# Optimization experiments

Hardware: AMD Instinct MI355X
Metric: run time of the kernel (lower is better)

## Reference

```python
import jax, jax.numpy as jnp
import numpy as np

N_HEAD = 16
HEAD_DIM = 64

def rotate_half(x):
    x1, x2 = jnp.split(x, 2, axis=-1)
    return jnp.concatenate((-x2, x1), axis=-1)

def rope_tables(T, dim):
    inv_freq = 1.0 / (10000.0 ** (jnp.arange(0, dim, 2, dtype=jnp.float32) / dim))
    t = jnp.arange(T, dtype=jnp.float32)
    freqs = jnp.einsum('i,j->ij', t, inv_freq)          # [T, dim/2]
    emb = jnp.concatenate((freqs, freqs), axis=-1)       # [T, dim]
    return jnp.cos(emb)[None, None], jnp.sin(emb)[None, None]  # [1,1,T,dim]

def setup_inputs() -> dict:
    key = jax.random.key(0)
    k1, k2, k3 = jax.random.split(key, 3)
    C = N_HEAD * HEAD_DIM
    x = jax.random.normal(k1, (2, 2048, C), dtype=jnp.float32)
    W_qkv = jax.random.normal(k2, (C, 3 * C), dtype=jnp.float32) * (1.0 / np.sqrt(C))
    W_proj = jax.random.normal(k3, (C, C), dtype=jnp.float32) * (1.0 / np.sqrt(C))
    return {"x": x, "W_qkv": W_qkv, "W_proj": W_proj}

def reference(x, W_qkv, W_proj):
    B, T, C = x.shape
    qkv = x @ W_qkv                                       # [B,T,3C]
    q, k, v = jnp.split(qkv, 3, axis=-1)
    def to_heads(a):
        return a.reshape(B, T, N_HEAD, HEAD_DIM).transpose(0, 2, 1, 3)  # [B,H,T,D]
    q, k, v = to_heads(q), to_heads(k), to_heads(v)
    cos, sin = rope_tables(T, HEAD_DIM)
    q = q * cos + rotate_half(q) * sin
    k = k * cos + rotate_half(k) * sin
    scale = 1.0 / jnp.sqrt(jnp.asarray(HEAD_DIM, dtype=x.dtype))
    scores = jnp.einsum('bhqd,bhkd->bhqk', q, k) * scale  # [B,H,T,T]
    causal = jnp.tril(jnp.ones((T, T), dtype=bool))
    scores = jnp.where(causal[None, None], scores, jnp.finfo(scores.dtype).min)
    attn = jax.nn.softmax(scores, axis=-1)
    out = jnp.einsum('bhqk,bhkd->bhqd', attn, v)          # [B,H,T,D]
    out = out.transpose(0, 2, 1, 3).reshape(B, T, C)
    return out @ W_proj
```

## Files before the change

kernel.cpp:

```cpp
#include <hip/hip_runtime.h>
#include <cstdint>
#include <cstddef>

typedef __attribute__((ext_vector_type(8))) short bf16x8;
typedef __attribute__((ext_vector_type(4))) float f32x4;

__device__ __forceinline__ unsigned short f2bf(float f) {
  unsigned int u = __builtin_bit_cast(unsigned int, f);
  u += 0x7FFFu + ((u >> 16) & 1u);
  return (unsigned short)(u >> 16);
}
__device__ __forceinline__ float bf2f(unsigned short h) {
  unsigned int u = ((unsigned int)h) << 16;
  return __builtin_bit_cast(float, u);
}

__device__ __forceinline__ void gl_lds16(const unsigned short* g, unsigned short* l) {
  __builtin_amdgcn_global_load_lds(
      (const __attribute__((address_space(1))) unsigned int*)(uintptr_t)g,
      (__attribute__((address_space(3))) unsigned int*)(unsigned int)(uintptr_t)l,
      16, 0, 0);
}

__global__ void k_prep(const float* __restrict__ x,
                       const float* __restrict__ Wqkv,
                       const float* __restrict__ Wproj,
                       unsigned short* __restrict__ xb,
                       unsigned short* __restrict__ wqt,
                       unsigned short* __restrict__ wpt,
                       float2* __restrict__ cstab) {
  __shared__ float tile[32][33];
  const int bid = blockIdx.x, tid = threadIdx.x;
  if (bid < 4096) {
    int i = bid * 256 + tid;
    float4 v = reinterpret_cast<const float4*>(x)[i];
    uint2 o;
    o.x = (unsigned int)f2bf(v.x) | ((unsigned int)f2bf(v.y) << 16);
    o.y = (unsigned int)f2bf(v.z) | ((unsigned int)f2bf(v.w) << 16);
    reinterpret_cast<uint2*>(xb)[i] = o;
  } else if (bid < 8192) {
    const float* in; unsigned short* out; int rows, cols, bx, by;
    if (bid < 7168) { in = Wqkv; out = wqt; rows = 1024; cols = 3072; bx = (bid - 4096) % 96; by = (bid - 4096) / 96; }
    else            { in = Wproj; out = wpt; rows = 1024; cols = 1024; bx = (bid - 7168) % 32; by = (bid - 7168) / 32; }
    int c0 = bx * 32, r0 = by * 32;
    int tx = tid & 31, ty = tid >> 5;
#pragma unroll
    for (int j = 0; j < 4; j++)
      tile[ty + j * 8][tx] = in[(size_t)(r0 + ty + j * 8) * cols + c0 + tx];
    __syncthreads();
#pragma unroll
    for (int j = 0; j < 4; j++)
      out[(size_t)(c0 + ty + j * 8) * rows + r0 + tx] = f2bf(tile[tx][ty + j * 8]);
  } else {
    int i = (bid - 8192) * 256 + tid;
    int t = i >> 5, j = i & 31;
    float invf = __powf(10000.0f, -(float)j / 32.0f);
    float ang = (float)t * invf;
    cstab[i] = make_float2(cosf(ang), sinf(ang));
  }
}

__global__ void k_gemm_qkv(const unsigned short* __restrict__ A,
                           const unsigned short* __restrict__ Bt,
                           const float2* __restrict__ cstab,
                           unsigned short* __restrict__ qh,
                           unsigned short* __restrict__ kh,
                           unsigned short* __restrict__ vt) {
  const int K = 1024;
  __shared__ unsigned short Ta[128 * 32];
  __shared__ unsigned short Tb[128 * 32];
  const int tid = threadIdx.x;
  const int bid0 = blockIdx.y * 24 + blockIdx.x;
  const int bid = (bid0 & 7) * 96 + (bid0 >> 3);
  const int m0 = (bid / 24) * 128, n0 = (bid % 24) * 128;
  const int w = tid >> 6, l = tid & 63;
  const int lr = l & 15, lg = l >> 4;
  const int wm = (w >> 1) * 64, wn = (w & 1) * 64;
  const int ssr = w * 32 + (l >> 2);
  const int ssc = (l & 3) * 8;
  unsigned short* ta0 = &Ta[w * 1024];
  unsigned short* tb0 = &Tb[w * 1024];
  f32x4 acc[4][4] = {};
  for (int k0 = 0; k0 < K; k0 += 32) {
    __syncthreads();
    gl_lds16(&A[(size_t)(m0 + ssr) * K + k0 + ssc],       ta0);
    gl_lds16(&A[(size_t)(m0 + ssr + 16) * K + k0 + ssc],  ta0 + 512);
    gl_lds16(&Bt[(size_t)(n0 + ssr) * K + k0 + ssc],      tb0);
    gl_lds16(&Bt[(size_t)(n0 + ssr + 16) * K + k0 + ssc], tb0 + 512);
    __syncthreads();
    bf16x8 af[4], bfr[4];
#pragma unroll
    for (int i = 0; i < 4; i++)
      af[i] = *(const bf16x8*)&Ta[(wm + i * 16 + lr) * 32 + lg * 8];
#pragma unroll
    for (int j = 0; j < 4; j++)
      bfr[j] = *(const bf16x8*)&Tb[(wn + j * 16 + lr) * 32 + lg * 8];
#pragma unroll
    for (int i = 0; i < 4; i++)
#pragma unroll
      for (int j = 0; j < 4; j++)
        acc[i][j] = __builtin_amdgcn_mfma_f32_16x16x32_bf16(af[i], bfr[j], acc[i][j], 0, 0, 0);
  }
  const int part = n0 >> 10;
  const int hbase = (n0 & 1023) + wn;
  if (part < 2) {
    unsigned short* dst = part ? kh : qh;
    const float scale = part ? 1.0f : 0.180336880111120420f;
#pragma unroll
    for (int i = 0; i < 4; i++) {
#pragma unroll
      for (int r = 0; r < 4; r++) {
        int gm = m0 + wm + i * 16 + lg * 4 + r;
        int t = gm & 2047, b = gm >> 11;
        float2 cs0 = cstab[t * 32 + lr];
        float2 cs1 = cstab[t * 32 + 16 + lr];
#pragma unroll
        for (int j = 0; j < 4; j++) {
          float val = acc[i][j][r];
          float par = acc[i][j ^ 2][r];
          float2 cs = (j & 1) ? cs1 : cs0;
          float out = (j < 2) ? (val * cs.x - par * cs.y)
                              : (val * cs.x + par * cs.y);
          int h = (hbase + j * 16) >> 6;
          int d = j * 16 + lr;
          int bh = b * 16 + h;
          dst[((size_t)(bh * 2048 + t)) * 64 + d] = f2bf(out * scale);
        }
      }
    }
  } else {
#pragma unroll
    for (int i = 0; i < 4; i++) {
      int tb = m0 + wm + i * 16 + lg * 4;
      int t0 = tb & 2047, b = tb >> 11;
#pragma unroll
      for (int j = 0; j < 4; j++) {
        int h = (hbase + j * 16) >> 6;
        int d = j * 16 + lr;
        int bh = b * 16 + h;
        unsigned short pv[4];
#pragma unroll
        for (int r = 0; r < 4; r++) pv[r] = f2bf(acc[i][j][r]);
        *(uint2*)&vt[((size_t)(bh * 64 + d)) * 2048 + t0] = *(uint2*)pv;
      }
    }
  }
}

__global__ void k_gemm_proj(const unsigned short* __restrict__ A,
                            const unsigned short* __restrict__ Bt,
                            float* __restrict__ C) {
  const int K = 1024;
  __shared__ unsigned short Ta[64 * 32];
  __shared__ unsigned short Tb[128 * 32];
  const int tid = threadIdx.x;
  const int bid0 = blockIdx.x;
  const int bid = (bid0 & 7) * 64 + (bid0 >> 3);
  const int n0 = (bid & 7) * 128;
  const int m0 = (bid >> 3) * 64;
  const int w = tid >> 6, l = tid & 63;
  const int lr = l & 15, lg = l >> 4;
  const int wn = w * 32;
  const int sra = tid >> 2, sca = (tid & 3) * 8;
  f32x4 acc[4][2] = {};
  for (int k0 = 0; k0 < K; k0 += 32) {
    __syncthreads();
    gl_lds16(&A[(size_t)(m0 + sra) * K + k0 + sca],        &Ta[tid * 8]);
    gl_lds16(&Bt[(size_t)(n0 + sra) * K + k0 + sca],       &Tb[tid * 8]);
    gl_lds16(&Bt[(size_t)(n0 + 64 + sra) * K + k0 + sca],  &Tb[(tid + 256) * 8]);
    __syncthreads();
    bf16x8 af[4], bfr[2];
#pragma unroll
    for (int i = 0; i < 4; i++)
      af[i] = *(const bf16x8*)&Ta[(i * 16 + lr) * 32 + lg * 8];
#pragma unroll
    for (int j = 0; j < 2; j++)
      bfr[j] = *(const bf16x8*)&Tb[(wn + j * 16 + lr) * 32 + lg * 8];
#pragma unroll
    for (int i = 0; i < 4; i++)
#pragma unroll
      for (int j = 0; j < 2; j++)
        acc[i][j] = __builtin_amdgcn_mfma_f32_16x16x32_bf16(af[i], bfr[j], acc[i][j], 0, 0, 0);
  }
#pragma unroll
  for (int i = 0; i < 4; i++)
#pragma unroll
    for (int j = 0; j < 2; j++)
#pragma unroll
      for (int r = 0; r < 4; r++)
        C[(size_t)(m0 + i * 16 + lg * 4 + r) * 1024 + n0 + wn + j * 16 + lr] = acc[i][j][r];
}

__global__ __launch_bounds__(256, 2) void k_attn(const unsigned short* __restrict__ qh,
                       const unsigned short* __restrict__ kh,
                       const unsigned short* __restrict__ vt,
                       unsigned short* __restrict__ att) {
  __shared__ unsigned short Kl[64 * 64];
  __shared__ unsigned short Vl[64 * 64];
  __shared__ unsigned short Pl[4][16 * 64];
  const int bid = blockIdx.x;
  const int bh  = ((bid & 7) << 2) | ((bid >> 3) >> 4);
  const int qt0 = (bid >> 3) & 15;
  const int qt1 = 31 - qt0;
  const int b = bh >> 4, h = bh & 15;
  const int tid = threadIdx.x;
  const int w = tid >> 6, l = tid & 63;
  const int lr = l & 15, lg = l >> 4;
  const unsigned short* qbase = qh + (size_t)bh * 2048 * 64;
  const unsigned short* kbase = kh + (size_t)bh * 2048 * 64;
  const unsigned short* vbase = vt + (size_t)bh * 64 * 2048;
  char* KB = (char*)Kl;
  char* VB = (char*)Vl;
  char* PB = (char*)&Pl[w][0];
  const int swz = (lr & 7) << 4;
  const int sr = tid >> 2, sc = (tid & 3) * 16;
  const int sb0 = (sr * 128 + sc * 2) ^ ((sr & 7) << 4);
  const int sb1 = (sr * 128 + sc * 2 + 16) ^ ((sr & 7) << 4);

  const int q00 = qt0 * 64, q01 = qt1 * 64;
  const int qrow0 = q00 + w * 16 + lr;
  const int qrow1 = q01 + w * 16 + lr;
  bf16x8 qa0 = *(const bf16x8*)&qbase[(size_t)qrow0 * 64 + lg * 8];
  bf16x8 qb0 = *(const bf16x8*)&qbase[(size_t)qrow0 * 64 + 32 + lg * 8];
  bf16x8 qa1 = *(const bf16x8*)&qbase[(size_t)qrow1 * 64 + lg * 8];
  bf16x8 qb1 = *(const bf16x8*)&qbase[(size_t)qrow1 * 64 + 32 + lg * 8];

  float mr0 = -3.0e38f, ls0 = 0.0f;
  float mr1 = -3.0e38f, ls1 = 0.0f;
  f32x4 of0[4] = {}, of1[4] = {};
  uint4 ka0, ka1, va0, va1;

  auto issue = [&](int kv0) {
    const unsigned short* ksrc = &kbase[(size_t)(kv0 + sr) * 64 + sc];
    const unsigned short* vsrc = &vbase[(size_t)sr * 2048 + kv0 + sc];
    ka0 = *(const uint4*)ksrc; ka1 = *(const uint4*)(ksrc + 8);
    va0 = *(const uint4*)vsrc; va1 = *(const uint4*)(vsrc + 8);
  };

  auto step = [&](f32x4 (&of)[4], float& mr, float& ls, bf16x8 qa, bf16x8 qb,
                  int qrow, int kv0, bool diag) {
    f32x4 s[4] = {};
    __builtin_amdgcn_s_setprio(1);
#pragma unroll
    for (int kq = 0; kq < 4; kq++) {
      bf16x8 kf0 = *(const bf16x8*)(KB + (((kq * 16 + lr) * 128 + lg * 16) ^ swz));
      bf16x8 kf1 = *(const bf16x8*)(KB + (((kq * 16 + lr) * 128 + 64 + lg * 16) ^ swz));
      s[kq] = __builtin_amdgcn_mfma_f32_16x16x32_bf16(kf0, qa, s[kq], 0, 0, 0);
      s[kq] = __builtin_amdgcn_mfma_f32_16x16x32_bf16(kf1, qb, s[kq], 0, 0, 0);
    }
    __builtin_amdgcn_s_setprio(0);
    if (diag) {
#pragma unroll
      for (int kq = 0; kq < 4; kq++)
#pragma unroll
        for (int r = 0; r < 4; r++)
          if (kv0 + kq * 16 + lg * 4 + r > qrow) s[kq][r] = -3.0e38f;
    }
    float pm = s[0][0];
#pragma unroll
    for (int kq = 0; kq < 4; kq++)
#pragma unroll
      for (int r = 0; r < 4; r++) pm = fmaxf(pm, s[kq][r]);
    pm = fmaxf(pm, __shfl_xor(pm, 16));
    pm = fmaxf(pm, __shfl_xor(pm, 32));
    float mnew = fmaxf(mr, pm);
    float alpha = __builtin_amdgcn_exp2f(mr - mnew);
    mr = mnew;
    float psum = 0.0f;
#pragma unroll
    for (int kq = 0; kq < 4; kq++)
#pragma unroll
      for (int r = 0; r < 4; r++) {
        float p = __builtin_amdgcn_exp2f(s[kq][r] - mnew);
        s[kq][r] = p;
        psum += p;
      }
    psum += __shfl_xor(psum, 16);
    psum += __shfl_xor(psum, 32);
    ls = ls * alpha + psum;
#pragma unroll
    for (int n = 0; n < 4; n++) {
      of[n][0] *= alpha; of[n][1] *= alpha; of[n][2] *= alpha; of[n][3] *= alpha;
    }
#pragma unroll
    for (int kq = 0; kq < 4; kq++) {
      uint2 pk;
      asm("v_cvt_pk_bf16_f32 %0, %1, %2" : "=v"(pk.x) : "v"(s[kq][0]), "v"(s[kq][1]));
      asm("v_cvt_pk_bf16_f32 %0, %1, %2" : "=v"(pk.y) : "v"(s[kq][2]), "v"(s[kq][3]));
      *(uint2*)(PB + ((lr * 128 + (kq * 16 + lg * 4) * 2) ^ swz)) = pk;
    }
    bf16x8 pb0 = *(const bf16x8*)(PB + ((lr * 128 + lg * 16) ^ swz));
    bf16x8 pb1 = *(const bf16x8*)(PB + ((lr * 128 + 64 + lg * 16) ^ swz));
    __builtin_amdgcn_s_setprio(1);
#pragma unroll
    for (int n = 0; n < 4; n++) {
      bf16x8 vf0 = *(const bf16x8*)(VB + (((n * 16 + lr) * 128 + lg * 16) ^ swz));
      bf16x8 vf1 = *(const bf16x8*)(VB + (((n * 16 + lr) * 128 + 64 + lg * 16) ^ swz));
      of[n] = __builtin_amdgcn_mfma_f32_16x16x32_bf16(vf0, pb0, of[n], 0, 0, 0);
      of[n] = __builtin_amdgcn_mfma_f32_16x16x32_bf16(vf1, pb1, of[n], 0, 0, 0);
    }
    __builtin_amdgcn_s_setprio(0);
  };

  issue(0);
  const int nkv0 = qt0 + 1;
  for (int s2 = 0; s2 < 33; s2++) {
    __syncthreads();
    *(uint4*)(KB + sb0) = ka0;  *(uint4*)(KB + sb1) = ka1;
    *(uint4*)(VB + sb0) = va0;  *(uint4*)(VB + sb1) = va1;
    __syncthreads();
    if (s2 < 32) {
      int ns = s2 + 1;
      issue(((ns < nkv0) ? ns : ns - nkv0) * 64);
    }
    if (s2 < nkv0) step(of0, mr0, ls0, qa0, qb0, qrow0, s2 * 64, s2 == qt0);
    else           step(of1, mr1, ls1, qa1, qb1, qrow1, (s2 - nkv0) * 64, s2 == 32);
  }

  auto store_half = [&](f32x4 (&of)[4], float ls, int q0) {
    float inv = 1.0f / ls;
#pragma unroll
    for (int n = 0; n < 4; n++) {
      uint2 pk;
      float o0 = of[n][0] * inv, o1 = of[n][1] * inv, o2 = of[n][2] * inv, o3 = of[n][3] * inv;
      asm("v_cvt_pk_bf16_f32 %0, %1, %2" : "=v"(pk.x) : "v"(o0), "v"(o1));
      asm("v_cvt_pk_bf16_f32 %0, %1, %2" : "=v"(pk.y) : "v"(o2), "v"(o3));
      *(uint2*)(PB + ((lr * 128 + (n * 16 + lg * 4) * 2) ^ swz)) = pk;
    }
    int r2 = l >> 2, c2 = (l & 3) * 16;
    int bo0 = (r2 * 128 + c2 * 2) ^ ((r2 & 7) << 4);
    int bo1 = (r2 * 128 + c2 * 2 + 16) ^ ((r2 & 7) << 4);
    uint4 o0 = *(const uint4*)(PB + bo0);
    uint4 o1 = *(const uint4*)(PB + bo1);
    unsigned short* orow = att + (size_t)(b * 2048 + q0 + w * 16 + r2) * 1024 + h * 64 + c2;
    *(uint4*)orow = o0;
    *(uint4*)(orow + 8) = o1;
  };
  store_half(of0, ls0, q00);
  store_half(of1, ls1, q01);
}

extern "C" void kernel_launch(void* const* d_in, const int* in_sizes, int n_in,
                              void* d_out, int out_size, void* d_ws, size_t ws_size,
                              hipStream_t stream) {
  const float* x     = (const float*)d_in[0];
  const float* Wqkv  = (const float*)d_in[1];
  const float* Wproj = (const float*)d_in[2];
  float* out = (float*)d_out;

  char* ws = (char*)d_ws;
  size_t off = 0;
  auto alloc = [&](size_t bytes) { void* p = ws + off; off += (bytes + 255) & ~(size_t)255; return p; };
  unsigned short* xb   = (unsigned short*)alloc((size_t)4096 * 1024 * 2);
  unsigned short* wqt  = (unsigned short*)alloc((size_t)3072 * 1024 * 2);
  unsigned short* wpt  = (unsigned short*)alloc((size_t)1024 * 1024 * 2);
  unsigned short* qh   = (unsigned short*)alloc((size_t)32 * 2048 * 64 * 2);
  unsigned short* kh   = (unsigned short*)alloc((size_t)32 * 2048 * 64 * 2);
  unsigned short* vt   = (unsigned short*)alloc((size_t)32 * 64 * 2048 * 2);
  unsigned short* att  = (unsigned short*)alloc((size_t)4096 * 1024 * 2);
  float2* cstab = (float2*)alloc((size_t)2048 * 32 * 8);

  k_prep<<<8448, 256, 0, stream>>>(x, Wqkv, Wproj, xb, wqt, wpt, cstab);
  k_gemm_qkv<<<dim3(24, 32), 256, 0, stream>>>(xb, wqt, cstab, qh, kh, vt);
  k_attn<<<512, 256, 0, stream>>>(qh, kh, vt, att);
  k_gemm_proj<<<512, 256, 0, stream>>>(att, wpt, out);
}
```

Measured before the change: 105.0 us.

## Restructure attention kernel around 32x32 MFMA tiles with double-buffered K/V

The attention kernel now gives each wave 32 query rows, so a block covers a 128-row query tile, and it uses 32x32x16 bf16 MFMAs in place of 16x16x32 ones. The P matrix is transposed in registers with permlane32_swap instead of a round trip through LDS. K/V tiles are double-buffered in LDS, cutting one of the two barriers per iteration. The online softmax skips rescaling the accumulators when the running max does not change. The query-tile-to-block mapping drops the old pairing of short and long causal tiles for a per-XCD ordering, which risks load imbalance and higher register pressure from the 16-wide accumulators.

```diff
diff --git a/kernel.cpp b/kernel.cpp
--- a/kernel.cpp
+++ b/kernel.cpp
@@ -4,6 +4,8 @@
 
 typedef __attribute__((ext_vector_type(8))) short bf16x8;
 typedef __attribute__((ext_vector_type(4))) float f32x4;
+typedef __attribute__((ext_vector_type(16))) float f32x16;
+typedef __attribute__((ext_vector_type(2))) unsigned int uint32x2;
 
 __device__ __forceinline__ unsigned short f2bf(float f) {
   unsigned int u = __builtin_bit_cast(unsigned int, f);
@@ -13,6 +15,11 @@
 __device__ __forceinline__ float bf2f(unsigned short h) {
   unsigned int u = ((unsigned int)h) << 16;
   return __builtin_bit_cast(float, u);
+}
+__device__ __forceinline__ unsigned cvtpk(float a, float b) {
+  unsigned r;
+  asm("v_cvt_pk_bf16_f32 %0, %1, %2" : "=v"(r) : "v"(a), "v"(b));
+  return r;
 }
 
 __device__ __forceinline__ void gl_lds16(const unsigned short* g, unsigned short* l) {
@@ -195,39 +202,35 @@
                        const unsigned short* __restrict__ kh,
                        const unsigned short* __restrict__ vt,
                        unsigned short* __restrict__ att) {
-  __shared__ unsigned short Kl[64 * 64];
-  __shared__ unsigned short Vl[64 * 64];
-  __shared__ unsigned short Pl[4][16 * 64];
+  __shared__ char SMEM[32768];
   const int bid = blockIdx.x;
-  const int bh  = ((bid & 7) << 2) | ((bid >> 3) >> 4);
-  const int qt0 = (bid >> 3) & 15;
-  const int qt1 = 31 - qt0;
+  const int xcd = bid & 7, u = bid >> 3;
+  int hl, qt;
+  if (u < 32) { hl = u >> 3; qt = u & 7; }
+  else        { hl = (u - 32) >> 3; qt = 15 - ((u - 32) & 7); }
+  const int bh = xcd * 4 + hl;
   const int b = bh >> 4, h = bh & 15;
   const int tid = threadIdx.x;
   const int w = tid >> 6, l = tid & 63;
-  const int lr = l & 15, lg = l >> 4;
+  const int lq = l & 31, g = l >> 5;
   const unsigned short* qbase = qh + (size_t)bh * 2048 * 64;
   const unsigned short* kbase = kh + (size_t)bh * 2048 * 64;
   const unsigned short* vbase = vt + (size_t)bh * 64 * 2048;
-  char* KB = (char*)Kl;
-  char* VB = (char*)Vl;
-  char* PB = (char*)&Pl[w][0];
-  const int swz = (lr & 7) << 4;
+  const int swz = (lq & 7) << 4;
   const int sr = tid >> 2, sc = (tid & 3) * 16;
   const int sb0 = (sr * 128 + sc * 2) ^ ((sr & 7) << 4);
   const int sb1 = (sr * 128 + sc * 2 + 16) ^ ((sr & 7) << 4);
 
-  const int q00 = qt0 * 64, q01 = qt1 * 64;
-  const int qrow0 = q00 + w * 16 + lr;
-  const int qrow1 = q01 + w * 16 + lr;
-  bf16x8 qa0 = *(const bf16x8*)&qbase[(size_t)qrow0 * 64 + lg * 8];
-  bf16x8 qb0 = *(const bf16x8*)&qbase[(size_t)qrow0 * 64 + 32 + lg * 8];
-  bf16x8 qa1 = *(const bf16x8*)&qbase[(size_t)qrow1 * 64 + lg * 8];
-  bf16x8 qb1 = *(const bf16x8*)&qbase[(size_t)qrow1 * 64 + 32 + lg * 8];
-
-  float mr0 = -3.0e38f, ls0 = 0.0f;
-  float mr1 = -3.0e38f, ls1 = 0.0f;
-  f32x4 of0[4] = {}, of1[4] = {};
+  const int q0 = qt * 128;
+  const int wq = q0 + 32 * w;
+  const int qrow = wq + lq;
+  bf16x8 qf[4];
+#pragma unroll
+  for (int dt = 0; dt < 4; dt++)
+    qf[dt] = *(const bf16x8*)&qbase[(size_t)qrow * 64 + dt * 16 + g * 8];
+
+  float mr = -3.0e38f, ls = 0.0f;
+  f32x16 of0 = {}, of1 = {};
   uint4 ka0, ka1, va0, va1;
 
   auto issue = [&](int kv0) {
@@ -237,107 +240,123 @@
     va0 = *(const uint4*)vsrc; va1 = *(const uint4*)(vsrc + 8);
   };
 
-  auto step = [&](f32x4 (&of)[4], float& mr, float& ls, bf16x8 qa, bf16x8 qb,
-                  int qrow, int kv0, bool diag) {
-    f32x4 s[4] = {};
-    __builtin_amdgcn_s_setprio(1);
-#pragma unroll
-    for (int kq = 0; kq < 4; kq++) {
-      bf16x8 kf0 = *(const bf16x8*)(KB + (((kq * 16 + lr) * 128 + lg * 16) ^ swz));
-      bf16x8 kf1 = *(const bf16x8*)(KB + (((kq * 16 + lr) * 128 + 64 + lg * 16) ^ swz));
-      s[kq] = __builtin_amdgcn_mfma_f32_16x16x32_bf16(kf0, qa, s[kq], 0, 0, 0);
-      s[kq] = __builtin_amdgcn_mfma_f32_16x16x32_bf16(kf1, qb, s[kq], 0, 0, 0);
-    }
-    __builtin_amdgcn_s_setprio(0);
-    if (diag) {
-#pragma unroll
-      for (int kq = 0; kq < 4; kq++)
-#pragma unroll
-        for (int r = 0; r < 4; r++)
-          if (kv0 + kq * 16 + lg * 4 + r > qrow) s[kq][r] = -3.0e38f;
-    }
-    float pm = s[0][0];
-#pragma unroll
-    for (int kq = 0; kq < 4; kq++)
-#pragma unroll
-      for (int r = 0; r < 4; r++) pm = fmaxf(pm, s[kq][r]);
-    pm = fmaxf(pm, __shfl_xor(pm, 16));
-    pm = fmaxf(pm, __shfl_xor(pm, 32));
-    float mnew = fmaxf(mr, pm);
-    float alpha = __builtin_amdgcn_exp2f(mr - mnew);
-    mr = mnew;
-    float psum = 0.0f;
-#pragma unroll
-    for (int kq = 0; kq < 4; kq++)
-#pragma unroll
-      for (int r = 0; r < 4; r++) {
-        float p = __builtin_amdgcn_exp2f(s[kq][r] - mnew);
-        s[kq][r] = p;
-        psum += p;
-      }
-    psum += __shfl_xor(psum, 16);
-    psum += __shfl_xor(psum, 32);
-    ls = ls * alpha + psum;
-#pragma unroll
-    for (int n = 0; n < 4; n++) {
-      of[n][0] *= alpha; of[n][1] *= alpha; of[n][2] *= alpha; of[n][3] *= alpha;
-    }
-#pragma unroll
-    for (int kq = 0; kq < 4; kq++) {
-      uint2 pk;
-      asm("v_cvt_pk_bf16_f32 %0, %1, %2" : "=v"(pk.x) : "v"(s[kq][0]), "v"(s[kq][1]));
-      asm("v_cvt_pk_bf16_f32 %0, %1, %2" : "=v"(pk.y) : "v"(s[kq][2]), "v"(s[kq][3]));
-      *(uint2*)(PB + ((lr * 128 + (kq * 16 + lg * 4) * 2) ^ swz)) = pk;
-    }
-    bf16x8 pb0 = *(const bf16x8*)(PB + ((lr * 128 + lg * 16) ^ swz));
-    bf16x8 pb1 = *(const bf16x8*)(PB + ((lr * 128 + 64 + lg * 16) ^ swz));
-    __builtin_amdgcn_s_setprio(1);
-#pragma unroll
-    for (int n = 0; n < 4; n++) {
-      bf16x8 vf0 = *(const bf16x8*)(VB + (((n * 16 + lr) * 128 + lg * 16) ^ swz));
-      bf16x8 vf1 = *(const bf16x8*)(VB + (((n * 16 + lr) * 128 + 64 + lg * 16) ^ swz));
-      of[n] = __builtin_amdgcn_mfma_f32_16x16x32_bf16(vf0, pb0, of[n], 0, 0, 0);
-      of[n] = __builtin_amdgcn_mfma_f32_16x16x32_bf16(vf1, pb1, of[n], 0, 0, 0);
-    }
-    __builtin_amdgcn_s_setprio(0);
-  };
-
+  const int nkv = 2 * qt + 2;
   issue(0);
-  const int nkv0 = qt0 + 1;
-  for (int s2 = 0; s2 < 33; s2++) {
-    __syncthreads();
-    *(uint4*)(KB + sb0) = ka0;  *(uint4*)(KB + sb1) = ka1;
-    *(uint4*)(VB + sb0) = va0;  *(uint4*)(VB + sb1) = va1;
-    __syncthreads();
-    if (s2 < 32) {
-      int ns = s2 + 1;
-      issue(((ns < nkv0) ? ns : ns - nkv0) * 64);
-    }
-    if (s2 < nkv0) step(of0, mr0, ls0, qa0, qb0, qrow0, s2 * 64, s2 == qt0);
-    else           step(of1, mr1, ls1, qa1, qb1, qrow1, (s2 - nkv0) * 64, s2 == 32);
-  }
-
-  auto store_half = [&](f32x4 (&of)[4], float ls, int q0) {
-    float inv = 1.0f / ls;
-#pragma unroll
-    for (int n = 0; n < 4; n++) {
-      uint2 pk;
-      float o0 = of[n][0] * inv, o1 = of[n][1] * inv, o2 = of[n][2] * inv, o3 = of[n][3] * inv;
-      asm("v_cvt_pk_bf16_f32 %0, %1, %2" : "=v"(pk.x) : "v"(o0), "v"(o1));
-      asm("v_cvt_pk_bf16_f32 %0, %1, %2" : "=v"(pk.y) : "v"(o2), "v"(o3));
-      *(uint2*)(PB + ((lr * 128 + (n * 16 + lg * 4) * 2) ^ swz)) = pk;
-    }
-    int r2 = l >> 2, c2 = (l & 3) * 16;
-    int bo0 = (r2 * 128 + c2 * 2) ^ ((r2 & 7) << 4);
-    int bo1 = (r2 * 128 + c2 * 2 + 16) ^ ((r2 & 7) << 4);
-    uint4 o0 = *(const uint4*)(PB + bo0);
-    uint4 o1 = *(const uint4*)(PB + bo1);
-    unsigned short* orow = att + (size_t)(b * 2048 + q0 + w * 16 + r2) * 1024 + h * 64 + c2;
-    *(uint4*)orow = o0;
-    *(uint4*)(orow + 8) = o1;
-  };
-  store_half(of0, ls0, q00);
-  store_half(of1, ls1, q01);
+  {
+    char* KB0 = SMEM;
+    char* VB0 = SMEM + 8192;
+    *(uint4*)(KB0 + sb0) = ka0;  *(uint4*)(KB0 + sb1) = ka1;
+    *(uint4*)(VB0 + sb0) = va0;  *(uint4*)(VB0 + sb1) = va1;
+  }
+  __syncthreads();
+
+  for (int t = 0; t < nkv; t++) {
+    const int kv0 = t * 64;
+    char* KBc = SMEM + (t & 1) * 16384;
+    char* VBc = KBc + 8192;
+    if (t + 1 < nkv) issue(kv0 + 64);
+    if (kv0 <= wq + 31) {
+      f32x16 s0 = {}, s1 = {};
+      __builtin_amdgcn_s_setprio(1);
+#pragma unroll
+      for (int dt = 0; dt < 4; dt++) {
+        bf16x8 k0 = *(const bf16x8*)(KBc + lq * 128 + ((dt * 32 + g * 16) ^ swz));
+        bf16x8 k1 = *(const bf16x8*)(KBc + (32 + lq) * 128 + ((dt * 32 + g * 16) ^ swz));
+        s0 = __builtin_amdgcn_mfma_f32_32x32x16_bf16(k0, qf[dt], s0, 0, 0, 0);
+        s1 = __builtin_amdgcn_mfma_f32_32x32x16_bf16(k1, qf[dt], s1, 0, 0, 0);
+      }
+      __builtin_amdgcn_s_setprio(0);
+      if (kv0 + 63 > wq) {
+#pragma unroll
+        for (int r = 0; r < 16; r++) {
+          int kk = kv0 + (r & 3) + 8 * (r >> 2) + 4 * g;
+          if (kk > qrow)      s0[r] = -3.0e38f;
+          if (kk + 32 > qrow) s1[r] = -3.0e38f;
+        }
+      }
+      float pm = s0[0];
+#pragma unroll
+      for (int r = 1; r < 16; r++) pm = fmaxf(pm, s0[r]);
+#pragma unroll
+      for (int r = 0; r < 16; r++) pm = fmaxf(pm, s1[r]);
+      pm = fmaxf(pm, __shfl_xor(pm, 32));
+      if (__all(pm <= mr)) {
+        float psum = 0.0f;
+#pragma unroll
+        for (int r = 0; r < 16; r++) { float p = __builtin_amdgcn_exp2f(s0[r] - mr); s0[r] = p; psum += p; }
+#pragma unroll
+        for (int r = 0; r < 16; r++) { float p = __builtin_amdgcn_exp2f(s1[r] - mr); s1[r] = p; psum += p; }
+        psum += __shfl_xor(psum, 32);
+        ls += psum;
+      } else {
+        float mnew = fmaxf(mr, pm);
+        float alpha = __builtin_amdgcn_exp2f(mr - mnew);
+        mr = mnew;
+        float psum = 0.0f;
+#pragma unroll
+        for (int r = 0; r < 16; r++) { float p = __builtin_amdgcn_exp2f(s0[r] - mnew); s0[r] = p; psum += p; }
+#pragma unroll
+        for (int r = 0; r < 16; r++) { float p = __builtin_amdgcn_exp2f(s1[r] - mnew); s1[r] = p; psum += p; }
+        psum += __shfl_xor(psum, 32);
+        ls = ls * alpha + psum;
+        of0 = of0 * alpha;
+        of1 = of1 * alpha;
+      }
+      bf16x8 pf[4];
+#pragma unroll
+      for (int kt = 0; kt < 2; kt++) {
+        f32x16& s = kt ? s1 : s0;
+        unsigned x0 = cvtpk(s[0], s[1]),   x1 = cvtpk(s[2], s[3]);
+        unsigned x2 = cvtpk(s[4], s[5]),   x3 = cvtpk(s[6], s[7]);
+        unsigned y0 = cvtpk(s[8], s[9]),   y1 = cvtpk(s[10], s[11]);
+        unsigned y2 = cvtpk(s[12], s[13]), y3 = cvtpk(s[14], s[15]);
+        uint32x2 r02 = __builtin_amdgcn_permlane32_swap(x0, x2, false, false);
+        uint32x2 r13 = __builtin_amdgcn_permlane32_swap(x1, x3, false, false);
+        uint32x2 t02 = __builtin_amdgcn_permlane32_swap(y0, y2, false, false);
+        uint32x2 t13 = __builtin_amdgcn_permlane32_swap(y1, y3, false, false);
+        uint4 pa, pb2;
+        pa.x = r02[0]; pa.y = r13[0]; pa.z = r02[1]; pa.w = r13[1];
+        pb2.x = t02[0]; pb2.y = t13[0]; pb2.z = t02[1]; pb2.w = t13[1];
+        pf[kt * 2]     = __builtin_bit_cast(bf16x8, pa);
+        pf[kt * 2 + 1] = __builtin_bit_cast(bf16x8, pb2);
+      }
+      __builtin_amdgcn_s_setprio(1);
+#pragma unroll
+      for (int ks = 0; ks < 4; ks++) {
+        bf16x8 v0 = *(const bf16x8*)(VBc + lq * 128 + ((ks * 32 + g * 16) ^ swz));
+        bf16x8 v1 = *(const bf16x8*)(VBc + (32 + lq) * 128 + ((ks * 32 + g * 16) ^ swz));
+        of0 = __builtin_amdgcn_mfma_f32_32x32x16_bf16(v0, pf[ks], of0, 0, 0, 0);
+        of1 = __builtin_amdgcn_mfma_f32_32x32x16_bf16(v1, pf[ks], of1, 0, 0, 0);
+      }
+      __builtin_amdgcn_s_setprio(0);
+    }
+    if (t + 1 < nkv) {
+      char* KBn = SMEM + ((t + 1) & 1) * 16384;
+      char* VBn = KBn + 8192;
+      *(uint4*)(KBn + sb0) = ka0;  *(uint4*)(KBn + sb1) = ka1;
+      *(uint4*)(VBn + sb0) = va0;  *(uint4*)(VBn + sb1) = va1;
+    }
+    __syncthreads();
+  }
+
+  char* SB = SMEM + w * 4096;
+  float inv = 1.0f / ls;
+#pragma unroll
+  for (int j = 0; j < 8; j++) {
+    int d0 = ((2 * j) & 3) + 8 * (j >> 1) + 4 * g;
+    *(unsigned*)(SB + ((lq * 128 + d0 * 2) ^ swz)) = cvtpk(of0[2 * j] * inv, of0[2 * j + 1] * inv);
+    *(unsigned*)(SB + ((lq * 128 + (32 + d0) * 2) ^ swz)) = cvtpk(of1[2 * j] * inv, of1[2 * j + 1] * inv);
+  }
+  {
+    int r2 = l >> 1, half = l & 1;
+    int X = (r2 & 7) << 4;
+    unsigned short* orow = att + (size_t)(b * 2048 + wq + r2) * 1024 + h * 64 + half * 32;
+#pragma unroll
+    for (int i = 0; i < 4; i++) {
+      uint4 o = *(const uint4*)(SB + ((r2 * 128 + half * 64 + i * 16) ^ X));
+      *(uint4*)(orow + i * 8) = o;
+    }
+  }
 }
 
 extern "C" void kernel_launch(void* const* d_in, const int* in_sizes, int n_in,
```

After: 115.0 us. +9.6%, slower.

## Double-buffer K/V tiles in LDS and skip rescale when running max unchanged

Applied to the files above, without the earlier changes.

The attention kernel now keeps two LDS buffers for K and V. The next tile is written into the alternate buffer after the current tile's compute, which cuts the per-iteration syncs from two to one. Separately, the online softmax checks wave-wide whether the block max exceeds the running max, and skips the alpha exp and the output rescale when it does not. LDS use grows to 40 KB per block, which may limit occupancy under launch_bounds(256,2), and the branch adds wave-uniform control flow.

```diff
diff --git a/kernel.cpp b/kernel.cpp
--- a/kernel.cpp
+++ b/kernel.cpp
@@ -195,9 +195,7 @@
                        const unsigned short* __restrict__ kh,
                        const unsigned short* __restrict__ vt,
                        unsigned short* __restrict__ att) {
-  __shared__ unsigned short Kl[64 * 64];
-  __shared__ unsigned short Vl[64 * 64];
-  __shared__ unsigned short Pl[4][16 * 64];
+  __shared__ char SMEM[40960];
   const int bid = blockIdx.x;
   const int bh  = ((bid & 7) << 2) | ((bid >> 3) >> 4);
   const int qt0 = (bid >> 3) & 15;
@@ -209,9 +207,7 @@
   const unsigned short* qbase = qh + (size_t)bh * 2048 * 64;
   const unsigned short* kbase = kh + (size_t)bh * 2048 * 64;
   const unsigned short* vbase = vt + (size_t)bh * 64 * 2048;
-  char* KB = (char*)Kl;
-  char* VB = (char*)Vl;
-  char* PB = (char*)&Pl[w][0];
+  char* PB = SMEM + 32768 + w * 2048;
   const int swz = (lr & 7) << 4;
   const int sr = tid >> 2, sc = (tid & 3) * 16;
   const int sb0 = (sr * 128 + sc * 2) ^ ((sr & 7) << 4);
@@ -238,7 +234,7 @@
   };
 
   auto step = [&](f32x4 (&of)[4], float& mr, float& ls, bf16x8 qa, bf16x8 qb,
-                  int qrow, int kv0, bool diag) {
+                  int qrow, int kv0, bool diag, char* KB, char* VB) {
     f32x4 s[4] = {};
     __builtin_amdgcn_s_setprio(1);
 #pragma unroll
@@ -263,24 +259,38 @@
       for (int r = 0; r < 4; r++) pm = fmaxf(pm, s[kq][r]);
     pm = fmaxf(pm, __shfl_xor(pm, 16));
     pm = fmaxf(pm, __shfl_xor(pm, 32));
-    float mnew = fmaxf(mr, pm);
-    float alpha = __builtin_amdgcn_exp2f(mr - mnew);
-    mr = mnew;
     float psum = 0.0f;
-#pragma unroll
-    for (int kq = 0; kq < 4; kq++)
-#pragma unroll
-      for (int r = 0; r < 4; r++) {
-        float p = __builtin_amdgcn_exp2f(s[kq][r] - mnew);
-        s[kq][r] = p;
-        psum += p;
+    if (__all(pm <= mr)) {
+#pragma unroll
+      for (int kq = 0; kq < 4; kq++)
+#pragma unroll
+        for (int r = 0; r < 4; r++) {
+          float p = __builtin_amdgcn_exp2f(s[kq][r] - mr);
+          s[kq][r] = p;
+          psum += p;
+        }
+      psum += __shfl_xor(psum, 16);
+      psum += __shfl_xor(psum, 32);
+      ls += psum;
+    } else {
+      float mnew = fmaxf(mr, pm);
+      float alpha = __builtin_amdgcn_exp2f(mr - mnew);
+      mr = mnew;
+#pragma unroll
+      for (int kq = 0; kq < 4; kq++)
+#pragma unroll
+        for (int r = 0; r < 4; r++) {
+          float p = __builtin_amdgcn_exp2f(s[kq][r] - mnew);
+          s[kq][r] = p;
+          psum += p;
+        }
+      psum += __shfl_xor(psum, 16);
+      psum += __shfl_xor(psum, 32);
+      ls = ls * alpha + psum;
+#pragma unroll
+      for (int n = 0; n < 4; n++) {
+        of[n][0] *= alpha; of[n][1] *= alpha; of[n][2] *= alpha; of[n][3] *= alpha;
       }
-    psum += __shfl_xor(psum, 16);
-    psum += __shfl_xor(psum, 32);
-    ls = ls * alpha + psum;
-#pragma unroll
-    for (int n = 0; n < 4; n++) {
-      of[n][0] *= alpha; of[n][1] *= alpha; of[n][2] *= alpha; of[n][3] *= alpha;
     }
 #pragma unroll
     for (int kq = 0; kq < 4; kq++) {
@@ -302,19 +312,32 @@
     __builtin_amdgcn_s_setprio(0);
   };
 
+  const int nkv0 = qt0 + 1;
   issue(0);
-  const int nkv0 = qt0 + 1;
+  {
+    char* KB0 = SMEM;
+    char* VB0 = SMEM + 16384;
+    *(uint4*)(KB0 + sb0) = ka0;  *(uint4*)(KB0 + sb1) = ka1;
+    *(uint4*)(VB0 + sb0) = va0;  *(uint4*)(VB0 + sb1) = va1;
+  }
+  __syncthreads();
+
   for (int s2 = 0; s2 < 33; s2++) {
-    __syncthreads();
-    *(uint4*)(KB + sb0) = ka0;  *(uint4*)(KB + sb1) = ka1;
-    *(uint4*)(VB + sb0) = va0;  *(uint4*)(VB + sb1) = va1;
-    __syncthreads();
     if (s2 < 32) {
       int ns = s2 + 1;
       issue(((ns < nkv0) ? ns : ns - nkv0) * 64);
     }
-    if (s2 < nkv0) step(of0, mr0, ls0, qa0, qb0, qrow0, s2 * 64, s2 == qt0);
-    else           step(of1, mr1, ls1, qa1, qb1, qrow1, (s2 - nkv0) * 64, s2 == 32);
+    char* KB = SMEM + (s2 & 1) * 8192;
+    char* VB = SMEM + 16384 + (s2 & 1) * 8192;
+    if (s2 < nkv0) step(of0, mr0, ls0, qa0, qb0, qrow0, s2 * 64, s2 == qt0, KB, VB);
+    else           step(of1, mr1, ls1, qa1, qb1, qrow1, (s2 - nkv0) * 64, s2 == 32, KB, VB);
+    if (s2 < 32) {
+      char* KBn = SMEM + ((s2 + 1) & 1) * 8192;
+      char* VBn = SMEM + 16384 + ((s2 + 1) & 1) * 8192;
+      *(uint4*)(KBn + sb0) = ka0;  *(uint4*)(KBn + sb1) = ka1;
+      *(uint4*)(VBn + sb0) = va0;  *(uint4*)(VBn + sb1) = va1;
+    }
+    __syncthreads();
   }
 
   auto store_half = [&](f32x4 (&of)[4], float ls, int q0) {
```

Result: slower. 107.1 us (+2.0%).

## Split paired causal query tiles into separate blocks with balanced scheduling order

Applied to the files above, without the earlier changes.

Each attention block previously handled two query tiles (qt and 31-qt) so that every block did 33 KV steps. Now each block handles one query tile, the grid doubles to 1024, and occupancy is raised to four blocks per CU. A per-XCD ordering interleaves long and short tiles so the load still balances. This trades perfectly balanced per-block work for more parallelism and fewer registers, at the risk of tail imbalance and more redundant K/V loads.

```diff
diff --git a/kernel.cpp b/kernel.cpp
--- a/kernel.cpp
+++ b/kernel.cpp
@@ -191,7 +191,7 @@
         C[(size_t)(m0 + i * 16 + lg * 4 + r) * 1024 + n0 + wn + j * 16 + lr] = acc[i][j][r];
 }
 
-__global__ __launch_bounds__(256, 2) void k_attn(const unsigned short* __restrict__ qh,
+__global__ __launch_bounds__(256, 4) void k_attn(const unsigned short* __restrict__ qh,
                        const unsigned short* __restrict__ kh,
                        const unsigned short* __restrict__ vt,
                        unsigned short* __restrict__ att) {
@@ -199,9 +199,14 @@
   __shared__ unsigned short Vl[64 * 64];
   __shared__ unsigned short Pl[4][16 * 64];
   const int bid = blockIdx.x;
-  const int bh  = ((bid & 7) << 2) | ((bid >> 3) >> 4);
-  const int qt0 = (bid >> 3) & 15;
-  const int qt1 = 31 - qt0;
+  const int xcd = bid & 7, u = bid >> 3;
+  const int hl = u >> 5, v = u & 31;
+  int qt;
+  if      (hl == 0) qt = v;
+  else if (hl == 1) qt = 31 - v;
+  else if (hl == 2) qt = (v + 16) & 31;
+  else              qt = (47 - v) & 31;
+  const int bh = xcd * 4 + hl;
   const int b = bh >> 4, h = bh & 15;
   const int tid = threadIdx.x;
   const int w = tid >> 6, l = tid & 63;
@@ -217,17 +222,13 @@
   const int sb0 = (sr * 128 + sc * 2) ^ ((sr & 7) << 4);
   const int sb1 = (sr * 128 + sc * 2 + 16) ^ ((sr & 7) << 4);
 
-  const int q00 = qt0 * 64, q01 = qt1 * 64;
-  const int qrow0 = q00 + w * 16 + lr;
-  const int qrow1 = q01 + w * 16 + lr;
-  bf16x8 qa0 = *(const bf16x8*)&qbase[(size_t)qrow0 * 64 + lg * 8];
-  bf16x8 qb0 = *(const bf16x8*)&qbase[(size_t)qrow0 * 64 + 32 + lg * 8];
-  bf16x8 qa1 = *(const bf16x8*)&qbase[(size_t)qrow1 * 64 + lg * 8];
-  bf16x8 qb1 = *(const bf16x8*)&qbase[(size_t)qrow1 * 64 + 32 + lg * 8];
-
-  float mr0 = -3.0e38f, ls0 = 0.0f;
-  float mr1 = -3.0e38f, ls1 = 0.0f;
-  f32x4 of0[4] = {}, of1[4] = {};
+  const int q0 = qt * 64;
+  const int qrow = q0 + w * 16 + lr;
+  bf16x8 qa = *(const bf16x8*)&qbase[(size_t)qrow * 64 + lg * 8];
+  bf16x8 qb = *(const bf16x8*)&qbase[(size_t)qrow * 64 + 32 + lg * 8];
+
+  float mr = -3.0e38f, ls = 0.0f;
+  f32x4 of[4] = {};
   uint4 ka0, ka1, va0, va1;
 
   auto issue = [&](int kv0) {
@@ -237,8 +238,15 @@
     va0 = *(const uint4*)vsrc; va1 = *(const uint4*)(vsrc + 8);
   };
 
-  auto step = [&](f32x4 (&of)[4], float& mr, float& ls, bf16x8 qa, bf16x8 qb,
-                  int qrow, int kv0, bool diag) {
+  issue(0);
+  for (int kb = 0; kb <= qt; kb++) {
+    const int kv0 = kb * 64;
+    __syncthreads();
+    *(uint4*)(KB + sb0) = ka0;  *(uint4*)(KB + sb1) = ka1;
+    *(uint4*)(VB + sb0) = va0;  *(uint4*)(VB + sb1) = va1;
+    __syncthreads();
+    if (kb < qt) issue((kb + 1) * 64);
+
     f32x4 s[4] = {};
     __builtin_amdgcn_s_setprio(1);
 #pragma unroll
@@ -249,7 +257,7 @@
       s[kq] = __builtin_amdgcn_mfma_f32_16x16x32_bf16(kf1, qb, s[kq], 0, 0, 0);
     }
     __builtin_amdgcn_s_setprio(0);
-    if (diag) {
+    if (kb == qt) {
 #pragma unroll
       for (int kq = 0; kq < 4; kq++)
 #pragma unroll
@@ -300,33 +308,18 @@
       of[n] = __builtin_amdgcn_mfma_f32_16x16x32_bf16(vf1, pb1, of[n], 0, 0, 0);
     }
     __builtin_amdgcn_s_setprio(0);
-  };
-
-  issue(0);
-  const int nkv0 = qt0 + 1;
-  for (int s2 = 0; s2 < 33; s2++) {
-    __syncthreads();
-    *(uint4*)(KB + sb0) = ka0;  *(uint4*)(KB + sb1) = ka1;
-    *(uint4*)(VB + sb0) = va0;  *(uint4*)(VB + sb1) = va1;
-    __syncthreads();
-    if (s2 < 32) {
-      int ns = s2 + 1;
-      issue(((ns < nkv0) ? ns : ns - nkv0) * 64);
-    }
-    if (s2 < nkv0) step(of0, mr0, ls0, qa0, qb0, qrow0, s2 * 64, s2 == qt0);
-    else           step(of1, mr1, ls1, qa1, qb1, qrow1, (s2 - nkv0) * 64, s2 == 32);
-  }
-
-  auto store_half = [&](f32x4 (&of)[4], float ls, int q0) {
-    float inv = 1.0f / ls;
-#pragma unroll
-    for (int n = 0; n < 4; n++) {
-      uint2 pk;
-      float o0 = of[n][0] * inv, o1 = of[n][1] * inv, o2 = of[n][2] * inv, o3 = of[n][3] * inv;
-      asm("v_cvt_pk_bf16_f32 %0, %1, %2" : "=v"(pk.x) : "v"(o0), "v"(o1));
-      asm("v_cvt_pk_bf16_f32 %0, %1, %2" : "=v"(pk.y) : "v"(o2), "v"(o3));
-      *(uint2*)(PB + ((lr * 128 + (n * 16 + lg * 4) * 2) ^ swz)) = pk;
-    }
+  }
+
+  float inv = 1.0f / ls;
+#pragma unroll
+  for (int n = 0; n < 4; n++) {
+    uint2 pk;
+    float o0 = of[n][0] * inv, o1 = of[n][1] * inv, o2 = of[n][2] * inv, o3 = of[n][3] * inv;
+    asm("v_cvt_pk_bf16_f32 %0, %1, %2" : "=v"(pk.x) : "v"(o0), "v"(o1));
+    asm("v_cvt_pk_bf16_f32 %0, %1, %2" : "=v"(pk.y) : "v"(o2), "v"(o3));
+    *(uint2*)(PB + ((lr * 128 + (n * 16 + lg * 4) * 2) ^ swz)) = pk;
+  }
+  {
     int r2 = l >> 2, c2 = (l & 3) * 16;
     int bo0 = (r2 * 128 + c2 * 2) ^ ((r2 & 7) << 4);
     int bo1 = (r2 * 128 + c2 * 2 + 16) ^ ((r2 & 7) << 4);
@@ -335,9 +328,7 @@
     unsigned short* orow = att + (size_t)(b * 2048 + q0 + w * 16 + r2) * 1024 + h * 64 + c2;
     *(uint4*)orow = o0;
     *(uint4*)(orow + 8) = o1;
-  };
-  store_half(of0, ls0, q00);
-  store_half(of1, ls1, q01);
+  }
 }
 
 extern "C" void kernel_launch(void* const* d_in, const int* in_sizes, int n_in,
@@ -362,6 +353,6 @@
 
   k_prep<<<8448, 256, 0, stream>>>(x, Wqkv, Wproj, xb, wqt, wpt, cstab);
   k_gemm_qkv<<<dim3(24, 32), 256, 0, stream>>>(xb, wqt, cstab, qh, kh, vt);
-  k_attn<<<512, 256, 0, stream>>>(qh, kh, vt, att);
+  k_attn<<<1024, 256, 0, stream>>>(qh, kh, vt, att);
   k_gemm_proj<<<512, 256, 0, stream>>>(att, wpt, out);
 }
```

Result: no change. 105.3 us (+0.3%).
